# Performance work log

Hardware: AMD Instinct MI355X
Metric: run time of the kernel (lower is better)

## Reference

```python
import jax, jax.numpy as jnp
import numpy as np

B, L, D_IN, D_GATE, D_HID, D_STATE = 4, 8192, 512, 2048, 128, 512
EPS = 1e-5


def _layernorm(x, g, b):
    m = jnp.mean(x, axis=-1, keepdims=True)
    v = jnp.var(x, axis=-1, keepdims=True)
    return (x - m) * jax.lax.rsqrt(v + EPS) * g + b


def _dss(u, g, b, lam_re, lam_im, c_re, c_im, d):
    # u: [B, L, H]; diagonal state-space mixing along L via FFT conv
    seq_len = u.shape[-2]
    un = _layernorm(u, g, b)
    residual = un * d                                   # learned skip, [B,L,H]
    lam = -jnp.exp(lam_re) + 1j * jnp.exp(lam_im)       # [N] complex
    c = (c_re + 1j * c_im) * (jnp.exp(lam) - 1.0) / lam  # [H,N]
    t = jnp.arange(seq_len, dtype=jnp.float32)
    s = jnp.exp(t[:, None] * lam[None, :])              # [L,N] Vandermonde
    kern = jnp.einsum('hn,ln->lh', c, s).real           # [L,H]
    n_fft = 2 * seq_len
    uf = jnp.fft.rfft(un, n=n_fft, axis=-2)             # [B, n_fft/2+1, H]
    kf = jnp.fft.rfft(kern, n=n_fft, axis=0)            # [n_fft/2+1, H]
    y = jnp.fft.irfft(uf * kf, n=n_fft, axis=-2)[..., :seq_len, :]
    return y + residual


def setup_inputs() -> dict:
    key = jax.random.key(0)
    ks = jax.random.split(key, 16)
    f32 = jnp.float32
    return {
        'x': jax.random.normal(ks[0], (B, L, D_IN), f32),
        'norm_g': jnp.ones((D_IN,), f32),
        'norm_b': jnp.zeros((D_IN,), f32),
        'W_v': jax.random.normal(ks[1], (D_GATE, D_IN), f32) / np.sqrt(D_IN),
        'W_u': jax.random.normal(ks[2], (D_HID, D_IN), f32) / np.sqrt(D_IN),
        'W_uc': jax.random.normal(ks[3], (D_GATE, D_HID), f32) / np.sqrt(D_HID),
        'W_o': jax.random.normal(ks[4], (D_IN, D_GATE), f32) / np.sqrt(D_GATE),
        'b_o': jnp.zeros((D_IN,), f32),
        'dss_g': jnp.ones((D_HID,), f32),
        'dss_b': jnp.zeros((D_HID,), f32),
        'lam_re': jax.random.normal(ks[5], (D_STATE,), f32),
        'lam_im': jax.random.normal(ks[6], (D_STATE,), f32),
        'C_re': jax.random.normal(ks[7], (D_HID, D_STATE), f32) / np.sqrt(D_STATE),
        'C_im': jax.random.normal(ks[8], (D_HID, D_STATE), f32) / np.sqrt(D_STATE),
        'D_skip': jax.random.normal(ks[9], (D_HID,), f32),
    }


def reference(x, norm_g, norm_b, W_v, W_u, W_uc, W_o, b_o,
              dss_g, dss_b, lam_re, lam_im, C_re, C_im, D_skip):
    xn = _layernorm(x, norm_g, norm_b)
    v = jax.nn.gelu(jnp.einsum('blf,gf->blg', xn, W_v), approximate=False)  # [B,L,G]
    u = jax.nn.gelu(jnp.einsum('blf,hf->blh', xn, W_u), approximate=False)  # [B,L,H]
    y = _dss(u, dss_g, dss_b, lam_re, lam_im, C_re, C_im, D_skip)           # [B,L,H]
    uc = jnp.einsum('blh,gh->blg', y, W_uc)                                 # [B,L,G]
    o = jnp.einsum('blg,fg->blf', uc * v, W_o) + b_o                        # [B,L,F]
    return o + x
```

## Files before the change

kernel.cpp:

```cpp
#include <hip/hip_runtime.h>
#include <math.h>
#include <stdint.h>

typedef unsigned short u16;
typedef unsigned int   u32;
typedef short short8 __attribute__((ext_vector_type(8)));
typedef float v4f    __attribute__((ext_vector_type(4)));

#define DEVI static __device__ __forceinline__

struct __align__(8)  U2 { u32 x, y; };
struct __align__(16) U4 { u32 x, y, z, w; };

static const int BB = 4, LL = 8192;
static const int BL = BB * LL;

DEVI float bf2f(u16 u){ u32 v = ((u32)u) << 16; float f; __builtin_memcpy(&f, &v, 4); return f; }
DEVI u16  f2bf(float f){ u32 u; __builtin_memcpy(&u, &f, 4); return (u16)((u + 0x7fffu + ((u >> 16) & 1u)) >> 16); }
DEVI float geluf(float x){ return 0.5f * x * (1.0f + erff(x * 0.7071067811865475f)); }

DEVI void ldsload16(const void* g, void* l){
  __builtin_amdgcn_global_load_lds(
      (const __attribute__((address_space(1))) u32*)(uintptr_t)g,
      (__attribute__((address_space(3)))  u32*)(u32)(uintptr_t)l,
      16, 0, 0);
}

__global__ __launch_bounds__(256) void k_cvt4(
    const float* __restrict__ s0, u16* __restrict__ d0, int n0,
    const float* __restrict__ s1, u16* __restrict__ d1, int n1,
    const float* __restrict__ s2, u16* __restrict__ d2, int n2,
    const float* __restrict__ s3, u16* __restrict__ d3, int n3){
  int i = blockIdx.x * 256 + threadIdx.x;
  if (i < n0){ d0[i] = f2bf(s0[i]); return; }
  i -= n0;
  if (i < n1){ d1[i] = f2bf(s1[i]); return; }
  i -= n1;
  if (i < n2){ d2[i] = f2bf(s2[i]); return; }
  i -= n2;
  if (i < n3){ d3[i] = f2bf(s3[i]); }
}

__global__ __launch_bounds__(256) void k_ln1(const float* __restrict__ x, const float* __restrict__ g,
                                             const float* __restrict__ b, u16* __restrict__ xn){
  int row = blockIdx.x, t = threadIdx.x;
  const float2* xr = (const float2*)(x + (int64_t)row * 512);
  float2 p = xr[t];
  float s = p.x + p.y, ss = p.x * p.x + p.y * p.y;
  for (int off = 32; off; off >>= 1){ s += __shfl_down(s, off); ss += __shfl_down(ss, off); }
  __shared__ float red[8];
  int w = t >> 6, lane = t & 63;
  if (!lane){ red[w] = s; red[4 + w] = ss; }
  __syncthreads();
  s  = red[0] + red[1] + red[2] + red[3];
  ss = red[4] + red[5] + red[6] + red[7];
  float m = s * (1.0f / 512.0f), var = ss * (1.0f / 512.0f) - m * m;
  float rs = rsqrtf(var + 1e-5f);
  float2 gv = ((const float2*)g)[t], bv = ((const float2*)b)[t];
  float r0 = (p.x - m) * rs * gv.x + bv.x;
  float r1 = (p.y - m) * rs * gv.y + bv.y;
  ((u32*)(xn + (int64_t)row * 512))[t] = (u32)f2bf(r0) | ((u32)f2bf(r1) << 16);
}

__global__ __launch_bounds__(256) void k_ln2(const u16* __restrict__ u, const float* __restrict__ g,
                                             const float* __restrict__ b, u16* __restrict__ un){
  int row = blockIdx.x * 4 + (threadIdx.x >> 6);
  int lane = threadIdx.x & 63;
  const u32* ur = (const u32*)(u + (int64_t)row * 128);
  u32 pv = ur[lane];
  float a = bf2f((u16)(pv & 0xffff)), c = bf2f((u16)(pv >> 16));
  float s = a + c, ss = a * a + c * c;
  for (int off = 32; off; off >>= 1){ s += __shfl_xor(s, off); ss += __shfl_xor(ss, off); }
  float m = s * (1.0f / 128.0f), var = ss * (1.0f / 128.0f) - m * m;
  float rs = rsqrtf(var + 1e-5f);
  float2 gv = ((const float2*)g)[lane], bv = ((const float2*)b)[lane];
  float r0 = (a - m) * rs * gv.x + bv.x;
  float r1 = (c - m) * rs * gv.y + bv.y;
  ((u32*)(un + (int64_t)row * 128))[lane] = (u32)f2bf(r0) | ((u32)f2bf(r1) << 16);
}

__global__ __launch_bounds__(256) void k_transpose(const u16* __restrict__ un, u16* __restrict__ unT){
  int bc = blockIdx.x >> 3, it = blockIdx.x & 7;
  int b = bc >> 4, cc = bc & 15;
  __shared__ __align__(16) u16 tile[64][128];
  const u16* src = un + ((int64_t)(b * 8192 + cc * 512 + it * 64)) * 128;
  int t = threadIdx.x;
  for (int p = 0; p < 4; p++){
    int id = p * 256 + t; int ri = id >> 4, seg = id & 15;
    *(U4*)&tile[ri][seg * 8] = *(const U4*)(src + (int64_t)ri * 128 + seg * 8);
  }
  __syncthreads();
  u16* dst = unT + ((int64_t)(bc * 128)) * 512 + it * 64;
  for (int p = 0; p < 4; p++){
    int id = p * 256 + t; int h = id >> 3, seg = id & 7;
    U4 pk; u16* pv = (u16*)&pk;
    for (int k2 = 0; k2 < 8; k2++) pv[k2] = tile[seg * 8 + k2][h];
    *(U4*)(dst + (int64_t)h * 512 + seg * 8) = pk;
  }
}

__global__ __launch_bounds__(512) void k_prep(const float* lam_re, const float* lam_im,
    const float* C_re, const float* C_im,
    u16* ZC, u16* PC, u16* VC, u16* ccat, float* cre, float* cim, float* zT){
  int n = blockIdx.x, t = threadIdx.x;
  float lr = -expf(lam_re[n]);
  float li =  expf(lam_im[n]);
  float mag = expf(lr * (float)t), ph = li * (float)t;
  float er = mag * cosf(ph), ei = mag * sinf(ph);
  ZC[(int64_t)n * 512 + (511 - t)]         = f2bf(er);
  ZC[(int64_t)(512 + n) * 512 + (511 - t)] = f2bf(ei);
  VC[(int64_t)t * 1024 + n]       = f2bf(er);
  VC[(int64_t)t * 1024 + 512 + n] = f2bf(-ei);
  float mag2 = expf(lr * (float)(t + 1)), ph2 = li * (float)(t + 1);
  PC[(int64_t)t * 1024 + n]       = f2bf(mag2 * cosf(ph2));
  PC[(int64_t)t * 1024 + 512 + n] = f2bf(-mag2 * sinf(ph2));
  if (t == 0){
    float m5 = expf(lr * 512.0f), p5 = li * 512.0f;
    zT[n] = m5 * cosf(p5); zT[512 + n] = m5 * sinf(p5);
  }
  if (t < 128){
    float e1m = expf(lr);
    float e1r = e1m * cosf(li), e1i = e1m * sinf(li);
    float nr = e1r - 1.0f, ni = e1i;
    float d2 = lr * lr + li * li;
    float qr = (nr * lr + ni * li) / d2, qi = (ni * lr - nr * li) / d2;
    float Cr = C_re[t * 512 + n], Ci = C_im[t * 512 + n];
    float vr = Cr * qr - Ci * qi, vi = Cr * qi + Ci * qr;
    cre[t * 512 + n] = vr; cim[t * 512 + n] = vi;
    ccat[(int64_t)t * 1024 + n] = f2bf(vr); ccat[(int64_t)t * 1024 + 512 + n] = f2bf(vi);
  }
}

__global__ __launch_bounds__(512) void k_rcat(const float* __restrict__ kern, u16* __restrict__ Rcat){
  int h = blockIdx.x >> 7, a = blockIdx.x & 127;
  int kcol = threadIdx.x;
  int d = 3 - (kcol >> 7);
  int delay = d * 128 + a - (kcol & 127);
  float val = (delay >= 0 && delay < 512) ? kern[delay * 128 + h] : 0.0f;
  Rcat[((int64_t)(h * 128 + a)) * 512 + kcol] = f2bf(val);
}

__global__ __launch_bounds__(256) void k_scan(const float* __restrict__ S, const float* __restrict__ cre,
    const float* __restrict__ cim, const float* __restrict__ zT, u16* __restrict__ WT){
  int tid = blockIdx.x * 256 + threadIdx.x;
  int n = tid & 511, bh = tid >> 9, b = bh >> 7, h = bh & 127;
  float cr = cre[h * 512 + n], ci = cim[h * 512 + n];
  float zr = zT[n], zi = zT[512 + n];
  float sR = 0.0f, sI = 0.0f;
  for (int cc = 0; cc < 16; cc++){
    int64_t m = (int64_t)(b * 16 + cc) * 128 + h;
    float wR = cr * sR - ci * sI, wI = cr * sI + ci * sR;
    WT[m * 1024 + n] = f2bf(wR);
    WT[m * 1024 + 512 + n] = f2bf(wI);
    float aR = S[m * 1024 + n], aI = S[m * 1024 + 512 + n];
    float nR = zr * sR - zi * sI + aR;
    sI = zr * sI + zi * sR + aI;
    sR = nR;
  }
}

__global__ __launch_bounds__(256) void k_assemble(const float* __restrict__ Yloc, const float* __restrict__ Ycross,
    const u16* __restrict__ un, const float* __restrict__ Dskip, u16* __restrict__ y){
  int64_t e = (int64_t)blockIdx.x * 256 + threadIdx.x;
  int h = (int)(e & 127); int64_t bl = e >> 7;
  int b = (int)(bl >> 13), l = (int)(bl & 8191);
  int cc = l >> 9, ii = l & 511, bc = b * 16 + cc;
  float val = Yloc[((int64_t)h * 512 + ii) * 64 + bc]
            + Ycross[(int64_t)ii * 8192 + (int64_t)bc * 128 + h]
            + bf2f(un[e]) * Dskip[h];
  y[e] = f2bf(val);
}

template<int EPI, bool TRI = false>
__global__ __launch_bounds__(256) void k_gemm(
    const u16* __restrict__ A, int64_t lda, int64_t aZ,
    const u16* __restrict__ B, int64_t ldb, int64_t bZ,
    void* Cp, int64_t ldc, int64_t cZ,
    int K, int Nvalid,
    const u16* aux1, const float* auxf1, const float* auxf2)
{
  __shared__ union __align__(16) SMU { u16 st[2][4096]; float ep[4][1088]; } sm;
  const int tid = threadIdx.x;
  const int lane = tid & 63, w = tid >> 6;
  const int wr = w >> 1, wc = w & 1, q = lane >> 4, c16 = lane & 15;
  const int sRow = lane >> 2, sSeg = lane & 3;
  const int z = blockIdx.z;

  int bx = blockIdx.x, by = blockIdx.y;
  if (!TRI && (gridDim.y & 7) == 0 && gridDim.x > 1){
    u32 idx = by * gridDim.x + bx;
    u32 xcd = idx & 7, s = idx >> 3;
    bx = s % gridDim.x;
    by = (s / gridDim.x) * 8 + xcd;
  }
  const int64_t m0 = (int64_t)by * 128;
  const int64_t n0 = (int64_t)bx * 128;

  const u16* Ab = A + (int64_t)z * aZ;
  const u16* Bp = B + (int64_t)z * bZ;
  int Keff = K;
  if (TRI){
    Ab += 384 - m0;
    Keff = (int)(m0 + 128);
  }

  v4f acc[4][4];
  #pragma unroll
  for (int i = 0; i < 4; i++)
    #pragma unroll
    for (int j = 0; j < 4; j++)
      acc[i][j] = (v4f)0.0f;

  for (int k0 = 0; k0 < Keff; k0 += 32){
    #pragma unroll
    for (int half = 0; half < 2; half++){
      int r0 = (half * 4 + w) * 16;
      int64_t arow = (TRI ? (int64_t)0 : m0) + r0 + sRow;
      ldsload16(Ab + arow * lda + k0 + sSeg * 8, &sm.st[0][r0 * 32]);
      int64_t brow = n0 + r0 + sRow;
      if (brow >= Nvalid) brow = Nvalid - 1;
      ldsload16(Bp + brow * ldb + k0 + sSeg * 8, &sm.st[1][r0 * 32]);
    }
    __syncthreads();
    short8 af[4], bfr[4];
    const u16* aB = &sm.st[0][(wr * 64 + c16) * 32 + q * 8];
    const u16* bB = &sm.st[1][(wc * 64 + c16) * 32 + q * 8];
    #pragma unroll
    for (int i = 0; i < 4; i++) af[i]  = *(const short8*)(aB + i * 512);
    #pragma unroll
    for (int j = 0; j < 4; j++) bfr[j] = *(const short8*)(bB + j * 512);
    #pragma unroll
    for (int i = 0; i < 4; i++)
      #pragma unroll
      for (int j = 0; j < 4; j++)
        acc[i][j] = __builtin_amdgcn_mfma_f32_16x16x32_bf16(af[i], bfr[j], acc[i][j], 0, 0, 0);
    __syncthreads();
  }

  if (EPI == 0 || EPI == 3){
    float* Cf = (float*)Cp + (int64_t)z * cZ;
    #pragma unroll
    for (int i = 0; i < 4; i++)
      #pragma unroll
      for (int j = 0; j < 4; j++){
        int64_t gr = m0 + wr * 64 + i * 16 + q * 4;
        int64_t gc = n0 + wc * 64 + j * 16 + c16;
        if (gc < Nvalid){
          #pragma unroll
          for (int r = 0; r < 4; r++){
            float vv = acc[i][j][r];
            if (EPI == 3) vv += auxf1[(gr + r) * ldc + gc] + auxf2[gc];
            Cf[(gr + r) * ldc + gc] = vv;
          }
        }
      }
    return;
  }

  u16* Cb = (u16*)Cp + (int64_t)z * cZ;
  float* ep = sm.ep[w];
  for (int i = 0; i < 4; i++){
    #pragma unroll
    for (int j = 0; j < 4; j++)
      #pragma unroll
      for (int r = 0; r < 4; r++){
        float vv = acc[i][j][r];
        if (EPI == 1) vv = geluf(vv);
        ep[(q * 4 + r) * 68 + j * 16 + c16] = vv;
      }
    #pragma unroll
    for (int p = 0; p < 4; p++){
      int id = p * 64 + lane;
      int row = id >> 4, cg = id & 15;
      float o0 = ep[row * 68 + cg * 4 + 0];
      float o1 = ep[row * 68 + cg * 4 + 1];
      float o2 = ep[row * 68 + cg * 4 + 2];
      float o3 = ep[row * 68 + cg * 4 + 3];
      int64_t gr = m0 + wr * 64 + i * 16 + row;
      int64_t gc = n0 + wc * 64 + cg * 4;
      if (EPI == 2){
        U2 pv = *(const U2*)(aux1 + gr * ldc + gc);
        o0 *= bf2f((u16)(pv.x & 0xffff)); o1 *= bf2f((u16)(pv.x >> 16));
        o2 *= bf2f((u16)(pv.y & 0xffff)); o3 *= bf2f((u16)(pv.y >> 16));
      }
      if (gc < Nvalid){
        U2 outp;
        outp.x = (u32)f2bf(o0) | ((u32)f2bf(o1) << 16);
        outp.y = (u32)f2bf(o2) | ((u32)f2bf(o3) << 16);
        *(U2*)(Cb + gr * ldc + gc) = outp;
      }
    }
  }
}

#define FENCE __builtin_amdgcn_sched_barrier(0)
#define BARX  __builtin_amdgcn_s_barrier()

#define STAGE(SRC, LD, TBASE, SEL, KT)                                          \
  { const u16* _g = (SRC) + (int64_t)(KT) * 64 + (int64_t)((SEL) * 128 + wid * 8) * (LD); \
    u16* _lb = (TBASE) + ((SEL) * 128 + wid * 8) * 64;                          \
    ldsload16(_g, _lb);                                                         \
    ldsload16(_g + (int64_t)64 * (LD), _lb + 64 * 64);                          \
  }

#define MFMAQ(QM, QN, BQ)                                                       \
  __builtin_amdgcn_s_setprio(1);                                                \
  _Pragma("unroll")                                                             \
  for (int mi = 0; mi < 4; mi++)                                                \
    _Pragma("unroll")                                                           \
    for (int ni = 0; ni < 2; ni++){                                             \
      acc[(QM)*4+mi][(QN)*2+ni] = __builtin_amdgcn_mfma_f32_16x16x32_bf16(      \
          af[mi][0], BQ[ni][0], acc[(QM)*4+mi][(QN)*2+ni], 0, 0, 0);            \
      acc[(QM)*4+mi][(QN)*2+ni] = __builtin_amdgcn_mfma_f32_16x16x32_bf16(      \
          af[mi][1], BQ[ni][1], acc[(QM)*4+mi][(QN)*2+ni], 0, 0, 0);            \
    }                                                                           \
  __builtin_amdgcn_s_setprio(0);

#define DO_TILE(T, BUFC, BUFN)                                                  \
  {                                                                             \
    const char* Ac = (const char*)(BUFC);                                       \
    const char* Bc = (const char*)((BUFC) + 16384);                             \
                \
    _Pragma("unroll")                                                           \
    for (int mi = 0; mi < 4; mi++){                                             \
      af[mi][0] = *(const short8*)(Ac + abase + mi * 2048 + kx0);               \
      af[mi][1] = *(const short8*)(Ac + abase + mi * 2048 + kx1);               \
    }                                                                           \
    _Pragma("unroll")                                                           \
    for (int ni = 0; ni < 2; ni++){                                             \
      bq0[ni][0] = *(const short8*)(Bc + bbase + ni * 2048 + kx0);              \
      bq0[ni][1] = *(const short8*)(Bc + bbase + ni * 2048 + kx1);              \
    }                                                                           \
    if ((T) + 1 < NT) STAGE(Bsrc, ldb, (BUFN) + 16384, 1, (T) + 1);             \
    FENCE; BARX; FENCE;                                                         \
    MFMAQ(0, 0, bq0);                                                           \
    FENCE; BARX; FENCE;                                                         \
        \
    _Pragma("unroll")                                                           \
    for (int ni = 0; ni < 2; ni++){                                             \
      bq1[ni][0] = *(const short8*)(Bc + 16384 + bbase + ni * 2048 + kx0);      \
      bq1[ni][1] = *(const short8*)(Bc + 16384 + bbase + ni * 2048 + kx1);      \
    }                                                                           \
    if ((T) + 2 < NT) STAGE(Asrc, lda, (BUFC), 0, (T) + 2);                     \
    FENCE; BARX; FENCE;                                                         \
    MFMAQ(0, 1, bq1);                                                           \
    FENCE; BARX; FENCE;                                                         \
          \
    _Pragma("unroll")                                                           \
    for (int mi = 0; mi < 4; mi++){                                             \
      af[mi][0] = *(const short8*)(Ac + 16384 + abase + mi * 2048 + kx0);       \
      af[mi][1] = *(const short8*)(Ac + 16384 + abase + mi * 2048 + kx1);       \
    }                                                                           \
    if ((T) + 2 < NT) STAGE(Bsrc, ldb, (BUFC) + 16384, 0, (T) + 2);             \
    FENCE; BARX; FENCE;                                                         \
    MFMAQ(1, 1, bq1);                                                           \
    FENCE; BARX; FENCE;                                                         \
         \
    if ((T) + 2 < NT){                                                          \
      STAGE(Asrc, lda, (BUFC), 1, (T) + 2);                                     \
      asm volatile("s_waitcnt vmcnt(6)" ::: "memory");                          \
    } else {                                                                    \
      asm volatile("s_waitcnt vmcnt(0)" ::: "memory");                          \
    }                                                                           \
    FENCE; BARX; FENCE;                                                         \
    MFMAQ(1, 0, bq0);                                                           \
    FENCE; BARX; FENCE;                                                         \
  }

__global__ __launch_bounds__(512) void k_gemm256(
    const u16* __restrict__ A, int64_t lda,
    const u16* __restrict__ B, int64_t ldb,
    float* __restrict__ C, int64_t ldc, int K,
    const float* __restrict__ auxf1, const float* __restrict__ auxf2)
{
  extern __shared__ __align__(16) u16 smd[];
  const int tid = threadIdx.x, wid = tid >> 6, lane = tid & 63;
  const int wr = wid >> 2, wc = wid & 3, c16 = lane & 15;

  int bx = blockIdx.x, by = blockIdx.y;
  if ((gridDim.y & 7) == 0 && gridDim.x > 1){
    u32 idx = by * gridDim.x + bx;
    u32 xcd = idx & 7, s = idx >> 3;
    bx = s % gridDim.x;
    by = (s / gridDim.x) * 8 + xcd;
  }
  const int64_t m0 = (int64_t)by * 256;
  const int64_t n0 = (int64_t)bx * 256;
  const int NT = K >> 6;

  const int rowin = lane >> 3;
  const int colel = 8 * ((lane & 7) ^ rowin);
  const u16* Asrc = A + (m0 + rowin) * lda + colel;
  const u16* Bsrc = B + (n0 + rowin) * ldb + colel;

  const int kx0 = ((lane >> 4) << 4) ^ ((lane & 7) << 4);
  const int kx1 = kx0 ^ 64;
  const int abase = (wr * 64 + c16) * 128;
  const int bbase = (wc * 32 + c16) * 128;

  u16* buf0 = smd;
  u16* buf1 = smd + 32768;

  v4f acc[8][4];
  #pragma unroll
  for (int i = 0; i < 8; i++)
    #pragma unroll
    for (int j = 0; j < 4; j++) acc[i][j] = (v4f)0.0f;

  short8 af[4][2], bq0[2][2], bq1[2][2];

  STAGE(Asrc, lda, buf0,         0, 0);
  STAGE(Bsrc, ldb, buf0 + 16384, 0, 0);
  STAGE(Bsrc, ldb, buf0 + 16384, 1, 0);
  STAGE(Asrc, lda, buf0,         1, 0);
  if (NT > 1){
    STAGE(Asrc, lda, buf1,         0, 1);
    STAGE(Bsrc, ldb, buf1 + 16384, 0, 1);
    STAGE(Asrc, lda, buf1,         1, 1);
    asm volatile("s_waitcnt vmcnt(6)" ::: "memory");
  } else {
    asm volatile("s_waitcnt vmcnt(0)" ::: "memory");
  }
  FENCE; BARX; FENCE;

  for (int t = 0; t < NT; t += 2){
    DO_TILE(t,     buf0, buf1)
    DO_TILE(t + 1, buf1, buf0)
  }

  const int q4 = (lane >> 4) << 2;
  #pragma unroll
  for (int qm = 0; qm < 2; qm++)
    #pragma unroll
    for (int mi = 0; mi < 4; mi++){
      int64_t gr = m0 + qm * 128 + wr * 64 + mi * 16 + q4;
      #pragma unroll
      for (int qn = 0; qn < 2; qn++)
        #pragma unroll
        for (int ni = 0; ni < 2; ni++){
          int64_t gc = n0 + qn * 128 + wc * 32 + ni * 16 + c16;
          v4f a = acc[qm * 4 + mi][qn * 2 + ni];
          float bo = auxf2[gc];
          #pragma unroll
          for (int r = 0; r < 4; r++)
            C[(gr + r) * ldc + gc] = a[r] + auxf1[(gr + r) * ldc + gc] + bo;
        }
    }
}

extern "C" void kernel_launch(void* const* d_in, const int* in_sizes, int n_in,
                              void* d_out, int out_size, void* d_ws, size_t ws_size,
                              hipStream_t stream) {
  (void)in_sizes; (void)n_in; (void)out_size; (void)ws_size;
  const float* x      = (const float*)d_in[0];
  const float* norm_g = (const float*)d_in[1];
  const float* norm_b = (const float*)d_in[2];
  const float* W_v    = (const float*)d_in[3];
  const float* W_u    = (const float*)d_in[4];
  const float* W_uc   = (const float*)d_in[5];
  const float* W_o    = (const float*)d_in[6];
  const float* b_o    = (const float*)d_in[7];
  const float* dss_g  = (const float*)d_in[8];
  const float* dss_b  = (const float*)d_in[9];
  const float* lam_re = (const float*)d_in[10];
  const float* lam_im = (const float*)d_in[11];
  const float* C_re   = (const float*)d_in[12];
  const float* C_im   = (const float*)d_in[13];
  const float* D_skip = (const float*)d_in[14];

  char* ob = (char*)d_out;
  u16* xn    = (u16*)(ob);
  u16* Wv_b  = (u16*)(ob + 33554432ull);
  u16* Wu_b  = (u16*)(ob + 35651584ull);

  char* ws = (char*)d_ws;
  const size_t R1      = 134217728ull;
  const size_t OFF_UN  = R1 + 33554432ull;
  const size_t OFF_UNT = OFF_UN + 8388608ull;
  const size_t OFF_R2  = OFF_UNT + 8388608ull;
  const size_t OFF_TAB = OFF_R2 + 33554432ull;

  u16*  v     = (u16*)(ws + 0);
  u16*  u     = (u16*)(ws + R1);
  u16*  Rcat  = (u16*)(ws + R1);
  u16*  WT    = (u16*)(ws + R1 + 16777216ull);
  u16*  un    = (u16*)(ws + OFF_UN);
  u16*  unT   = (u16*)(ws + OFF_UNT);
  u16*  y     = (u16*)(ws + OFF_UNT);
  float* S    = (float*)(ws + OFF_R2);
  float* Ycross = (float*)(ws + OFF_R2);
  float* Yloc = (float*)(ws + OFF_R2 + 16777216ull);
  char* tp = ws + OFF_TAB;
  u16*  ZC   = (u16*)tp;            tp += 1048576;
  u16*  PC   = (u16*)tp;            tp += 1048576;
  u16*  VC   = (u16*)tp;            tp += 1048576;
  u16*  ccat = (u16*)tp;            tp += 262144;
  float* cre = (float*)tp;          tp += 262144;
  float* cim = (float*)tp;          tp += 262144;
  float* zT  = (float*)tp;          tp += 4096;
  float* kern= (float*)tp;          tp += 262144;
  u16*  Wo_b = (u16*)tp;            tp += 2097152;
  u16*  Wuc_b= (u16*)tp;            tp += 524288;

  k_cvt4<<<9472, 256, 0, stream>>>(W_v, Wv_b, 2048 * 512,
                                   W_u, Wu_b, 128 * 512,
                                   W_uc, Wuc_b, 2048 * 128,
                                   W_o, Wo_b, 512 * 2048);

  k_ln1<<<BL, 256, 0, stream>>>(x, norm_g, norm_b, xn);
  k_prep<<<512, 512, 0, stream>>>(lam_re, lam_im, C_re, C_im, ZC, PC, VC, ccat, cre, cim, zT);

  k_gemm<1><<<dim3(16, 256, 1), 256, 0, stream>>>(xn, 512, 0, Wv_b, 512, 0, v, 2048, 0, 512, 2048, nullptr, nullptr, nullptr);
  k_gemm<1><<<dim3(1, 256, 1), 256, 0, stream>>>(xn, 512, 0, Wu_b, 512, 0, u, 128, 0, 512, 128, nullptr, nullptr, nullptr);
  k_ln2<<<BL / 4, 256, 0, stream>>>(u, dss_g, dss_b, un);
  k_transpose<<<512, 256, 0, stream>>>(un, unT);

  k_gemm<0><<<dim3(1, 4, 1), 256, 0, stream>>>(VC, 1024, 0, ccat, 1024, 0, kern, 128, 0, 1024, 128, nullptr, nullptr, nullptr);
  k_rcat<<<16384, 512, 0, stream>>>(kern, Rcat);

  k_gemm<0><<<dim3(8, 64, 1), 256, 0, stream>>>(unT, 512, 0, ZC, 512, 0, S, 1024, 0, 512, 1024, nullptr, nullptr, nullptr);
  k_scan<<<1024, 256, 0, stream>>>(S, cre, cim, zT, WT);
  k_gemm<0><<<dim3(64, 4, 1), 256, 0, stream>>>(PC, 1024, 0, WT, 1024, 0, Ycross, 8192, 0, 1024, 8192, nullptr, nullptr, nullptr);
  k_gemm<0, true><<<dim3(1, 4, 128), 256, 0, stream>>>(
      Rcat, 512, 65536, unT, 65536, 512, Yloc, 64, 32768, 512, 64, nullptr, nullptr, nullptr);
  k_assemble<<<16384, 256, 0, stream>>>(Yloc, Ycross, un, D_skip, y);

  k_gemm<2><<<dim3(16, 256, 1), 256, 0, stream>>>(y, 128, 0, Wuc_b, 128, 0, v, 2048, 0, 128, 2048, v, nullptr, nullptr);
  k_gemm256<<<dim3(2, 128), 512, 131072, stream>>>(v, 2048, Wo_b, 2048, (float*)d_out, 512, 2048, x, b_o);
}
```

Baseline: 667.8 us.

## Route gate GEMMs through 256x256 pipelined kernel with bf16 epilogues and fast GELU

Templates the 256x256 LDS-pipelined GEMM on epilogue type, adding a GELU bf16-output epilogue and a multiply-by-aux bf16 epilogue. Both run through a per-wave LDS scratch so each lane writes 16-byte vectors. The W_v projection and the W_uc gating GEMM move from the 128-tile kernel to this larger-tile kernel, which gives more reuse per block. The erf-based GELU is replaced by an Abramowitz-Stegun polynomial using hardware rcp/exp2, which trades a small accuracy loss for cheaper transcendentals. The dead EPI 2/3 paths are removed from the old kernel.

```diff
diff --git a/kernel.cpp b/kernel.cpp
--- a/kernel.cpp
+++ b/kernel.cpp
@@ -17,7 +17,17 @@
 
 DEVI float bf2f(u16 u){ u32 v = ((u32)u) << 16; float f; __builtin_memcpy(&f, &v, 4); return f; }
 DEVI u16  f2bf(float f){ u32 u; __builtin_memcpy(&u, &f, 4); return (u16)((u + 0x7fffu + ((u >> 16) & 1u)) >> 16); }
-DEVI float geluf(float x){ return 0.5f * x * (1.0f + erff(x * 0.7071067811865475f)); }
+
+DEVI float geluf(float x){
+  float z = fabsf(x) * 0.7071067811865475f;
+  float t = __builtin_amdgcn_rcpf(1.0f + 0.3275911f * z);
+  float p = t * (0.254829592f + t * (-0.284496736f + t * (1.421413741f +
+            t * (-1.453152027f + t * 1.061405429f))));
+  float e = __builtin_amdgcn_exp2f(z * z * -1.4426950408889634f);
+  float er = 1.0f - p * e;
+  float s = (x < 0.0f) ? -er : er;
+  return 0.5f * x * (1.0f + s);
+}
 
 DEVI void ldsload16(const void* g, void* l){
   __builtin_amdgcn_global_load_lds(
@@ -237,7 +247,7 @@
     __syncthreads();
   }
 
-  if (EPI == 0 || EPI == 3){
+  if (EPI == 0){
     float* Cf = (float*)Cp + (int64_t)z * cZ;
     #pragma unroll
     for (int i = 0; i < 4; i++)
@@ -247,11 +257,8 @@
         int64_t gc = n0 + wc * 64 + j * 16 + c16;
         if (gc < Nvalid){
           #pragma unroll
-          for (int r = 0; r < 4; r++){
-            float vv = acc[i][j][r];
-            if (EPI == 3) vv += auxf1[(gr + r) * ldc + gc] + auxf2[gc];
-            Cf[(gr + r) * ldc + gc] = vv;
-          }
+          for (int r = 0; r < 4; r++)
+            Cf[(gr + r) * ldc + gc] = acc[i][j][r];
         }
       }
     return;
@@ -278,11 +285,6 @@
       float o3 = ep[row * 68 + cg * 4 + 3];
       int64_t gr = m0 + wr * 64 + i * 16 + row;
       int64_t gc = n0 + wc * 64 + cg * 4;
-      if (EPI == 2){
-        U2 pv = *(const U2*)(aux1 + gr * ldc + gc);
-        o0 *= bf2f((u16)(pv.x & 0xffff)); o1 *= bf2f((u16)(pv.x >> 16));
-        o2 *= bf2f((u16)(pv.y & 0xffff)); o3 *= bf2f((u16)(pv.y >> 16));
-      }
       if (gc < Nvalid){
         U2 outp;
         outp.x = (u32)f2bf(o0) | ((u32)f2bf(o1) << 16);
@@ -320,7 +322,6 @@
   {                                                                             \
     const char* Ac = (const char*)(BUFC);                                       \
     const char* Bc = (const char*)((BUFC) + 16384);                             \
-                \
     _Pragma("unroll")                                                           \
     for (int mi = 0; mi < 4; mi++){                                             \
       af[mi][0] = *(const short8*)(Ac + abase + mi * 2048 + kx0);               \
@@ -335,7 +336,6 @@
     FENCE; BARX; FENCE;                                                         \
     MFMAQ(0, 0, bq0);                                                           \
     FENCE; BARX; FENCE;                                                         \
-        \
     _Pragma("unroll")                                                           \
     for (int ni = 0; ni < 2; ni++){                                             \
       bq1[ni][0] = *(const short8*)(Bc + 16384 + bbase + ni * 2048 + kx0);      \
@@ -345,7 +345,6 @@
     FENCE; BARX; FENCE;                                                         \
     MFMAQ(0, 1, bq1);                                                           \
     FENCE; BARX; FENCE;                                                         \
-          \
     _Pragma("unroll")                                                           \
     for (int mi = 0; mi < 4; mi++){                                             \
       af[mi][0] = *(const short8*)(Ac + 16384 + abase + mi * 2048 + kx0);       \
@@ -355,7 +354,6 @@
     FENCE; BARX; FENCE;                                                         \
     MFMAQ(1, 1, bq1);                                                           \
     FENCE; BARX; FENCE;                                                         \
-         \
     if ((T) + 2 < NT){                                                          \
       STAGE(Asrc, lda, (BUFC), 1, (T) + 2);                                     \
       asm volatile("s_waitcnt vmcnt(6)" ::: "memory");                          \
@@ -367,15 +365,18 @@
     FENCE; BARX; FENCE;                                                         \
   }
 
+template<int EPI>
 __global__ __launch_bounds__(512) void k_gemm256(
     const u16* __restrict__ A, int64_t lda,
     const u16* __restrict__ B, int64_t ldb,
-    float* __restrict__ C, int64_t ldc, int K,
+    void* __restrict__ Cp, int64_t ldc, int K,
+    const u16* __restrict__ aux1,
     const float* __restrict__ auxf1, const float* __restrict__ auxf2)
 {
   extern __shared__ __align__(16) u16 smd[];
   const int tid = threadIdx.x, wid = tid >> 6, lane = tid & 63;
   const int wr = wid >> 2, wc = wid & 3, c16 = lane & 15;
+  const int q4 = (lane >> 4) << 2;
 
   int bx = blockIdx.x, by = blockIdx.y;
   if ((gridDim.y & 7) == 0 && gridDim.x > 1){
@@ -428,24 +429,63 @@
     DO_TILE(t + 1, buf1, buf0)
   }
 
-  const int q4 = (lane >> 4) << 2;
+  if (EPI == 0){
+    float* C = (float*)Cp;
+    #pragma unroll
+    for (int qm = 0; qm < 2; qm++)
+      #pragma unroll
+      for (int mi = 0; mi < 4; mi++){
+        int64_t gr = m0 + qm * 128 + wr * 64 + mi * 16 + q4;
+        #pragma unroll
+        for (int qn = 0; qn < 2; qn++)
+          #pragma unroll
+          for (int ni = 0; ni < 2; ni++){
+            int64_t gc = n0 + qn * 128 + wc * 32 + ni * 16 + c16;
+            v4f a = acc[qm * 4 + mi][qn * 2 + ni];
+            float bo = auxf2[gc];
+            #pragma unroll
+            for (int r = 0; r < 4; r++)
+              C[(gr + r) * ldc + gc] = a[r] + auxf1[(gr + r) * ldc + gc] + bo;
+          }
+      }
+    return;
+  }
+
+  u16* Cb = (u16*)Cp;
+  float* scr = (float*)smd + wid * 528;
+  const int erow = lane >> 2, eseg = lane & 3;
   #pragma unroll
   for (int qm = 0; qm < 2; qm++)
     #pragma unroll
-    for (int mi = 0; mi < 4; mi++){
-      int64_t gr = m0 + qm * 128 + wr * 64 + mi * 16 + q4;
+    for (int mi = 0; mi < 4; mi++)
       #pragma unroll
-      for (int qn = 0; qn < 2; qn++)
+      for (int qn = 0; qn < 2; qn++){
         #pragma unroll
         for (int ni = 0; ni < 2; ni++){
-          int64_t gc = n0 + qn * 128 + wc * 32 + ni * 16 + c16;
           v4f a = acc[qm * 4 + mi][qn * 2 + ni];
-          float bo = auxf2[gc];
           #pragma unroll
-          for (int r = 0; r < 4; r++)
-            C[(gr + r) * ldc + gc] = a[r] + auxf1[(gr + r) * ldc + gc] + bo;
+          for (int r = 0; r < 4; r++){
+            float vv = a[r];
+            if (EPI == 1) vv = geluf(vv);
+            scr[(q4 + r) * 33 + ni * 16 + c16] = vv;
+          }
         }
-    }
+        float o[8];
+        #pragma unroll
+        for (int kq = 0; kq < 8; kq++) o[kq] = scr[erow * 33 + eseg * 8 + kq];
+        int64_t gr = m0 + qm * 128 + wr * 64 + mi * 16 + erow;
+        int64_t gc = n0 + qn * 128 + wc * 32 + eseg * 8;
+        if (EPI == 2){
+          U4 pv = *(const U4*)(aux1 + gr * ldc + gc);
+          const u16* pp = (const u16*)&pv;
+          #pragma unroll
+          for (int kq = 0; kq < 8; kq++) o[kq] *= bf2f(pp[kq]);
+        }
+        U4 outp; u16* op = (u16*)&outp;
+        #pragma unroll
+        for (int kq = 0; kq < 8; kq++) op[kq] = f2bf(o[kq]);
+        *(U4*)(Cb + gr * ldc + gc) = outp;
+      }
 }
 
 extern "C" void kernel_launch(void* const* d_in, const int* in_sizes, int n_in,
@@ -510,7 +550,7 @@
   k_ln1<<<BL, 256, 0, stream>>>(x, norm_g, norm_b, xn);
   k_prep<<<512, 512, 0, stream>>>(lam_re, lam_im, C_re, C_im, ZC, PC, VC, ccat, cre, cim, zT);
 
-  k_gemm<1><<<dim3(16, 256, 1), 256, 0, stream>>>(xn, 512, 0, Wv_b, 512, 0, v, 2048, 0, 512, 2048, nullptr, nullptr, nullptr);
+  k_gemm256<1><<<dim3(8, 128), 512, 131072, stream>>>(xn, 512, Wv_b, 512, v, 2048, 512, nullptr, nullptr, nullptr);
   k_gemm<1><<<dim3(1, 256, 1), 256, 0, stream>>>(xn, 512, 0, Wu_b, 512, 0, u, 128, 0, 512, 128, nullptr, nullptr, nullptr);
   k_ln2<<<BL / 4, 256, 0, stream>>>(u, dss_g, dss_b, un);
   k_transpose<<<512, 256, 0, stream>>>(un, unT);
@@ -525,6 +565,6 @@
       Rcat, 512, 65536, unT, 65536, 512, Yloc, 64, 32768, 512, 64, nullptr, nullptr, nullptr);
   k_assemble<<<16384, 256, 0, stream>>>(Yloc, Ycross, un, D_skip, y);
 
-  k_gemm<2><<<dim3(16, 256, 1), 256, 0, stream>>>(y, 128, 0, Wuc_b, 128, 0, v, 2048, 0, 128, 2048, v, nullptr, nullptr);
-  k_gemm256<<<dim3(2, 128), 512, 131072, stream>>>(v, 2048, Wo_b, 2048, (float*)d_out, 512, 2048, x, b_o);
-}
+  k_gemm256<2><<<dim3(8, 128), 512, 131072, stream>>>(y, 128, Wuc_b, 128, v, 2048, 128, v, nullptr, nullptr);
+  k_gemm256<0><<<dim3(2, 128), 512, 131072, stream>>>(v, 2048, Wo_b, 2048, d_out, 512, 2048, nullptr, x, b_o);
+}
```

Result: faster. 590.1 us (-11.6%).
